# Performance work log

Measured on AMD Instinct MI355X. Metric: run time of the kernel, lower is better.

## Reference

```python
import jax, jax.numpy as jnp
import numpy as np

OUT_FEATURES = 4096
IN_FEATURES = 4096


def _unpack_int4_symmetric(packed, n_values):
    # packed: uint8-valued int32 array; each byte holds two 4-bit values:
    # high nibble first, low nibble second (packing was (v0 << 4) | v1 with v in [0,15]=q+8)
    high = (packed >> 4) & 15
    low = packed & 15
    interleaved = jnp.stack([high, low], axis=-1).reshape(-1)[:n_values]
    # symmetric: quantized value q = nibble - 8, zero_point = 0
    return interleaved.astype(jnp.float32) - 8.0


def setup_inputs() -> dict:
    key = jax.random.key(0)
    k1, k2, k3, k4, k5 = jax.random.split(key, 5)
    x = jax.random.normal(k1, (4, 2048, IN_FEATURES), dtype=jnp.float32)
    packed_w = jax.random.randint(k2, (OUT_FEATURES * IN_FEATURES // 2,), 0, 256, dtype=jnp.int32)
    packed_b = jax.random.randint(k3, (OUT_FEATURES // 2,), 0, 256, dtype=jnp.int32)
    scale_w = jax.random.uniform(k4, (), dtype=jnp.float32) * 0.01 + 1e-4
    scale_b = jax.random.uniform(k5, (), dtype=jnp.float32) * 0.01 + 1e-4
    return {"x": x, "packed_w": packed_w, "packed_b": packed_b,
            "scale_w": scale_w, "scale_b": scale_b}


def reference(x, packed_w, packed_b, scale_w, scale_b):
    # dequantize weight: scale * (q - zero_point), zero_point = 0 (symmetric)
    qw = _unpack_int4_symmetric(packed_w, OUT_FEATURES * IN_FEATURES)
    W = (scale_w * qw).reshape(OUT_FEATURES, IN_FEATURES)  # [O, I]
    qb = _unpack_int4_symmetric(packed_b, OUT_FEATURES)
    b = scale_b * qb  # [O]
    # F.linear(x, W, b) = x @ W.T + b
    return jnp.einsum('bsi,oi->bso', x, W) + b
```

## Files before the change

### kernel.cpp

```cpp
#include <hip/hip_runtime.h>

#define M_DIM 8192
#define N_DIM 4096
#define K_DIM 4096

typedef _Float16 f16;
typedef _Float16 f16x8 __attribute__((ext_vector_type(8)));
typedef float f32x16 __attribute__((ext_vector_type(16)));

__device__ __forceinline__ void lds_async16(void* lds, const void* g) {
    __builtin_amdgcn_global_load_lds(
        (const __attribute__((address_space(1))) void*)(void*)g,
        (__attribute__((address_space(3))) void*)lds, 16, 0, 0);
}

__global__ __launch_bounds__(256) void cvt_x_kernel(const float* __restrict__ x, f16* __restrict__ xh) {
    size_t idx  = (size_t)blockIdx.x * 256 + threadIdx.x;
    size_t base = idx * 8;
    const float4* xp = (const float4*)(x + base);
    float4 v0 = xp[0], v1 = xp[1];
    f16x8 h;
    h[0] = (f16)v0.x; h[1] = (f16)v0.y; h[2] = (f16)v0.z; h[3] = (f16)v0.w;
    h[4] = (f16)v1.x; h[5] = (f16)v1.y; h[6] = (f16)v1.z; h[7] = (f16)v1.w;
    *(f16x8*)(xh + base) = h;
}

__global__ __launch_bounds__(256) void cvt_w_kernel(const int* __restrict__ pw, f16* __restrict__ wh) {
    size_t idx = (size_t)blockIdx.x * 256 + threadIdx.x;
    int4 v = ((const int4*)pw)[idx];
    f16x8 h;
    int a;
    a = v.x; h[0] = (f16)(((a >> 4) & 15) - 8); h[1] = (f16)((a & 15) - 8);
    a = v.y; h[2] = (f16)(((a >> 4) & 15) - 8); h[3] = (f16)((a & 15) - 8);
    a = v.z; h[4] = (f16)(((a >> 4) & 15) - 8); h[5] = (f16)((a & 15) - 8);
    a = v.w; h[6] = (f16)(((a >> 4) & 15) - 8); h[7] = (f16)((a & 15) - 8);
    *(f16x8*)(wh + idx * 8) = h;
}

__global__ __launch_bounds__(512, 2) void gemm_f16(const f16* __restrict__ A, const f16* __restrict__ B,
                                                   const int* __restrict__ pb,
                                                   const float* __restrict__ psw, const float* __restrict__ psb,
                                                   float* __restrict__ out) {
    __shared__ f16 As[2][16384];
    __shared__ f16 Bs[2][16384];

    const int tid  = threadIdx.x;
    const int wave = tid >> 6;
    const int lane = tid & 63;
    const int l32  = lane & 31;
    const int half = lane >> 5;
    const int wm   = wave >> 2;
    const int wn   = wave & 3;

    const int bid = blockIdx.x;
    const int swz = (bid & 7) * 64 + (bid >> 3);
    const int bx  = swz & 15;
    const int by  = swz >> 4;
    const int mbase = by * 256;
    const int nbase = bx * 256;

    const int rL   = ((lane >> 5) & 1) * 8 + ((lane >> 2) & 7);
    const int kswz = (((lane & 3) ^ ((lane >> 3) & 3))) * 8;
    const f16* aSrc[2]; const f16* bSrc[2];
#pragma unroll
    for (int j = 0; j < 2; j++) {
        aSrc[j] = A + (size_t)(mbase + j * 128 + wave * 16 + rL) * K_DIM + kswz;
        bSrc[j] = B + (size_t)(nbase + j * 128 + wave * 16 + rL) * K_DIM + kswz;
    }
    const int dA0 = wave * 512;
    const int dA1 = 4096 + wave * 512;

    int aoff[4], axr[4];
#pragma unroll
    for (int mt = 0; mt < 4; mt++) {
        int ra = wm * 128 + mt * 32 + l32;
        aoff[mt] = (ra >> 3) * 256 + (ra & 7) * 32;
        axr[mt]  = ((ra & 7) >> 1) & 3;
    }
    int boff[2], bxr[2];
#pragma unroll
    for (int nt = 0; nt < 2; nt++) {
        int rb = wn * 64 + nt * 32 + l32;
        boff[nt] = (rb >> 3) * 256 + (rb & 7) * 32;
        bxr[nt]  = ((rb & 7) >> 1) & 3;
    }

    f32x16 acc[4][2] = {};

    lds_async16(&As[0][dA0], aSrc[0]);
    lds_async16(&As[0][dA1], aSrc[1]);
    lds_async16(&Bs[0][dA0], bSrc[0]);
    lds_async16(&Bs[0][dA1], bSrc[1]);
    lds_async16(&As[0][8192 + dA0], aSrc[0] + 32);
    lds_async16(&As[0][8192 + dA1], aSrc[1] + 32);
    lds_async16(&Bs[0][8192 + dA0], bSrc[0] + 32);
    lds_async16(&Bs[0][8192 + dA1], bSrc[1] + 32);
    asm volatile("s_waitcnt vmcnt(0)" ::: "memory");
    __builtin_amdgcn_s_barrier();

#pragma unroll 1
    for (int t = 0; t < 64; ++t) {
        const f16* Ac = As[t & 1];
        const f16* Bc = Bs[t & 1];
        f16* An = As[(t + 1) & 1];
        f16* Bn = Bs[(t + 1) & 1];
        const int kn = (t < 63 ? (t + 1) : 63) * 64;

        lds_async16(&An[dA0], aSrc[0] + kn);
        lds_async16(&An[dA1], aSrc[1] + kn);
        lds_async16(&Bn[dA0], bSrc[0] + kn);
        lds_async16(&Bn[dA1], bSrc[1] + kn);
        lds_async16(&An[8192 + dA0], aSrc[0] + kn + 32);
        lds_async16(&An[8192 + dA1], aSrc[1] + kn + 32);
        lds_async16(&Bn[8192 + dA0], bSrc[0] + kn + 32);
        lds_async16(&Bn[8192 + dA1], bSrc[1] + kn + 32);
        __builtin_amdgcn_sched_barrier(0);

#pragma unroll
        for (int kk = 0; kk < 4; ++kk) {
            const int h_   = kk >> 1;
            const int kc2_ = (kk & 1) * 2 + half;
            f16x8 af[4], bf[2];
#pragma unroll
            for (int mt = 0; mt < 4; mt++)
                af[mt] = *(const f16x8*)&Ac[h_ * 8192 + aoff[mt] + ((kc2_ ^ axr[mt]) << 3)];
#pragma unroll
            for (int nt = 0; nt < 2; nt++)
                bf[nt] = *(const f16x8*)&Bc[h_ * 8192 + boff[nt] + ((kc2_ ^ bxr[nt]) << 3)];
#pragma unroll
            for (int mt = 0; mt < 4; mt++)
#pragma unroll
                for (int nt = 0; nt < 2; nt++)
                    acc[mt][nt] = __builtin_amdgcn_mfma_f32_32x32x16_f16(af[mt], bf[nt], acc[mt][nt], 0, 0, 0);
        }

        asm volatile("s_waitcnt vmcnt(0)" ::: "memory");
        __builtin_amdgcn_s_barrier();
        __builtin_amdgcn_sched_barrier(0);
    }

    const float sw = *psw;
    const float sb = *psb;

#pragma unroll
    for (int nt = 0; nt < 2; nt++) {
        const int gcol = nbase + wn * 64 + nt * 32 + l32;
        const int p    = pb[gcol >> 1];
        const int nib  = (gcol & 1) ? (p & 15) : ((p >> 4) & 15);
        const float bias = sb * (float)(nib - 8);
#pragma unroll
        for (int mt = 0; mt < 4; mt++) {
            const int rbase = mbase + wm * 128 + mt * 32 + half * 4;
#pragma unroll
            for (int g = 0; g < 4; g++) {
                float* o = out + (size_t)(rbase + g * 8) * N_DIM + gcol;
#pragma unroll
                for (int r = 0; r < 4; r++)
                    o[(size_t)r * N_DIM] = sw * acc[mt][nt][g * 4 + r] + bias;
            }
        }
    }
}

__global__ __launch_bounds__(256) void gemm_fallback(const float* __restrict__ x, const int* __restrict__ pw,
                                                     const int* __restrict__ pb,
                                                     const float* __restrict__ psw, const float* __restrict__ psb,
                                                     float* __restrict__ out) {
    __shared__ float As[16][17];
    __shared__ float Bs[16][17];
    const int tx = threadIdx.x & 15, ty = threadIdx.x >> 4;
    const int row = blockIdx.y * 16 + ty;
    const int col = blockIdx.x * 16 + tx;
    float acc = 0.f;
    for (int k0 = 0; k0 < K_DIM; k0 += 16) {
        As[ty][tx] = x[(size_t)row * K_DIM + k0 + tx];
        const int nrow = blockIdx.x * 16 + ty;
        const int k = k0 + tx;
        const int p = pw[((size_t)nrow * K_DIM + k) >> 1];
        const int nib = (k & 1) ? (p & 15) : ((p >> 4) & 15);
        Bs[ty][tx] = (float)(nib - 8);
        __syncthreads();
#pragma unroll
        for (int kk = 0; kk < 16; kk++)
            acc += As[ty][kk] * Bs[tx][kk];
        __syncthreads();
    }
    const float sw = *psw, sb = *psb;
    const int p = pb[col >> 1];
    const int nib = (col & 1) ? (p & 15) : ((p >> 4) & 15);
    out[(size_t)row * N_DIM + col] = sw * acc + sb * (float)(nib - 8);
}

extern "C" void kernel_launch(void* const* d_in, const int* in_sizes, int n_in,
                              void* d_out, int out_size, void* d_ws, size_t ws_size,
                              hipStream_t stream) {
    (void)in_sizes; (void)n_in; (void)out_size;
    const float* x   = (const float*)d_in[0];
    const int*   pw  = (const int*)d_in[1];
    const int*   pb  = (const int*)d_in[2];
    const float* psw = (const float*)d_in[3];
    const float* psb = (const float*)d_in[4];
    float* out = (float*)d_out;

    const size_t xh_bytes = (size_t)M_DIM * K_DIM * sizeof(f16);
    const size_t wh_bytes = (size_t)N_DIM * K_DIM * sizeof(f16);

    if (ws_size >= xh_bytes + wh_bytes) {
        f16* xh = (f16*)d_ws;
        f16* wh = (f16*)((char*)d_ws + xh_bytes);
        cvt_x_kernel<<<(M_DIM * (size_t)K_DIM) / 8 / 256, 256, 0, stream>>>(x, xh);
        cvt_w_kernel<<<((size_t)N_DIM * K_DIM / 2) / 4 / 256, 256, 0, stream>>>(pw, wh);
        gemm_f16<<<dim3((M_DIM / 256) * (N_DIM / 256)), 512, 0, stream>>>(xh, wh, pb, psw, psb, out);
    } else {
        gemm_fallback<<<dim3(N_DIM / 16, M_DIM / 16), 256, 0, stream>>>(x, pw, pb, psw, psb, out);
    }
}
```

Measured before the change: 541.3 us.

## Restructure f16 GEMM main loop into four-phase pipelined schedule with 16x16 MFMA

Rewrites the GEMM inner loop to use 16x16x32 MFMA tiles and splits each K step into four quadrant phases. Global-to-LDS loads for the next tiles are interleaved between phases, with barriers and s_setprio raising priority around the MFMA bursts. Loads are issued per half-tile kind so copies overlap compute at a finer grain. Out-of-range stages load into a scratch buffer to keep vmcnt counts uniform. This adds more barriers per iteration and relies on exact waitcnt accounting, which could stall or be fragile.

```diff
diff --git a/kernel.cpp b/kernel.cpp
--- a/kernel.cpp
+++ b/kernel.cpp
@@ -6,7 +6,7 @@
 
 typedef _Float16 f16;
 typedef _Float16 f16x8 __attribute__((ext_vector_type(8)));
-typedef float f32x16 __attribute__((ext_vector_type(16)));
+typedef float f32x4 __attribute__((ext_vector_type(4)));
 
 __device__ __forceinline__ void lds_async16(void* lds, const void* g) {
     __builtin_amdgcn_global_load_lds(
@@ -41,16 +41,18 @@
                                                    const int* __restrict__ pb,
                                                    const float* __restrict__ psw, const float* __restrict__ psb,
                                                    float* __restrict__ out) {
-    __shared__ f16 As[2][16384];
-    __shared__ f16 Bs[2][16384];
+    __shared__ f16 AS[2][2][8192];
+    __shared__ f16 BS[2][2][8192];
+    __shared__ f16 SCR[1024];
 
     const int tid  = threadIdx.x;
-    const int wave = tid >> 6;
+    const int w    = tid >> 6;
     const int lane = tid & 63;
-    const int l32  = lane & 31;
-    const int half = lane >> 5;
-    const int wm   = wave >> 2;
-    const int wn   = wave & 3;
+    const int l16  = lane & 15;
+    const int lq   = lane >> 4;
+    const int wm   = w >> 2;
+    const int wn   = w & 3;
+    const int hb   = wn >> 1;
 
     const int bid = blockIdx.x;
     const int swz = (bid & 7) * 64 + (bid >> 3);
@@ -59,107 +61,166 @@
     const int mbase = by * 256;
     const int nbase = bx * 256;
 
-    const int rL   = ((lane >> 5) & 1) * 8 + ((lane >> 2) & 7);
-    const int kswz = (((lane & 3) ^ ((lane >> 3) & 3))) * 8;
-    const f16* aSrc[2]; const f16* bSrc[2];
-#pragma unroll
-    for (int j = 0; j < 2; j++) {
-        aSrc[j] = A + (size_t)(mbase + j * 128 + wave * 16 + rL) * K_DIM + kswz;
-        bSrc[j] = B + (size_t)(nbase + j * 128 + wave * 16 + rL) * K_DIM + kswz;
-    }
-    const int dA0 = wave * 512;
-    const int dA1 = 4096 + wave * 512;
-
-    int aoff[4], axr[4];
-#pragma unroll
-    for (int mt = 0; mt < 4; mt++) {
-        int ra = wm * 128 + mt * 32 + l32;
-        aoff[mt] = (ra >> 3) * 256 + (ra & 7) * 32;
-        axr[mt]  = ((ra & 7) >> 1) & 3;
-    }
-    int boff[2], bxr[2];
-#pragma unroll
-    for (int nt = 0; nt < 2; nt++) {
-        int rb = wn * 64 + nt * 32 + l32;
-        boff[nt] = (rb >> 3) * 256 + (rb & 7) * 32;
-        bxr[nt]  = ((rb & 7) >> 1) & 3;
-    }
-
-    f32x16 acc[4][2] = {};
-
-    lds_async16(&As[0][dA0], aSrc[0]);
-    lds_async16(&As[0][dA1], aSrc[1]);
-    lds_async16(&Bs[0][dA0], bSrc[0]);
-    lds_async16(&Bs[0][dA1], bSrc[1]);
-    lds_async16(&As[0][8192 + dA0], aSrc[0] + 32);
-    lds_async16(&As[0][8192 + dA1], aSrc[1] + 32);
-    lds_async16(&Bs[0][8192 + dA0], bSrc[0] + 32);
-    lds_async16(&Bs[0][8192 + dA1], bSrc[1] + 32);
+    const int uL = (lane & 7) ^ (((lane >> 5) & 1) << 1);
+    const f16* aSrc00 = A + (size_t)(mbase + w * 16 + (lane >> 3)) * K_DIM + uL * 8;
+    const f16* aSrc01 = aSrc00 + (size_t)8 * K_DIM;
+    const f16* aSrc10 = aSrc00 + (size_t)128 * K_DIM;
+    const f16* aSrc11 = aSrc10 + (size_t)8 * K_DIM;
+    const f16* bSrc00 = B + (size_t)(nbase + w * 16 + (lane >> 3)) * K_DIM + uL * 8;
+    const f16* bSrc01 = bSrc00 + (size_t)8 * K_DIM;
+    const f16* bSrc10 = bSrc00 + (size_t)128 * K_DIM;
+    const f16* bSrc11 = bSrc10 + (size_t)8 * K_DIM;
+    const int wb = w * 1024;
+
+#define STAGE_KIND(tidx, kind) do {                                                              \
+    if ((tidx) < 64) {                                                                           \
+        const int b_ = (tidx) & 1;                                                               \
+        if ((kind) == 0) { lds_async16(&AS[b_][0][wb], aSrc00 + (tidx) * 64);                    \
+                           lds_async16(&AS[b_][0][wb + 512], aSrc01 + (tidx) * 64); }            \
+        else if ((kind) == 1) { lds_async16(&BS[b_][0][wb], bSrc00 + (tidx) * 64);               \
+                                lds_async16(&BS[b_][0][wb + 512], bSrc01 + (tidx) * 64); }       \
+        else if ((kind) == 2) { lds_async16(&AS[b_][1][wb], aSrc10 + (tidx) * 64);               \
+                                lds_async16(&AS[b_][1][wb + 512], aSrc11 + (tidx) * 64); }       \
+        else { lds_async16(&BS[b_][1][wb], bSrc10 + (tidx) * 64);                                \
+               lds_async16(&BS[b_][1][wb + 512], bSrc11 + (tidx) * 64); }                        \
+    } else {                                                                                     \
+        lds_async16(&SCR[0], aSrc00 + 4032); lds_async16(&SCR[512], aSrc01 + 4032);              \
+    }                                                                                            \
+} while (0)
+
+    int aAd[2][4];
+#pragma unroll
+    for (int mq = 0; mq < 2; mq++)
+#pragma unroll
+        for (int fi = 0; fi < 4; fi++) {
+            const int r  = mq * 64 + fi * 16 + l16;
+            const int xr = ((r >> 2) & 1) << 1;
+            aAd[mq][fi]  = r * 64 + ((lq ^ xr) << 3);
+        }
+    int bAd[2][2];
+#pragma unroll
+    for (int nq = 0; nq < 2; nq++)
+#pragma unroll
+        for (int gi = 0; gi < 2; gi++) {
+            const int r  = (wn & 1) * 64 + nq * 32 + gi * 16 + l16;
+            const int xr = ((r >> 2) & 1) << 1;
+            bAd[nq][gi]  = r * 64 + ((lq ^ xr) << 3);
+        }
+
+    f32x4 acc[8][4] = {};
+
+    STAGE_KIND(0, 0); STAGE_KIND(0, 1); STAGE_KIND(0, 2); STAGE_KIND(0, 3);
+    STAGE_KIND(1, 1); STAGE_KIND(1, 0);
+    asm volatile("s_waitcnt vmcnt(4)" ::: "memory");
+    __builtin_amdgcn_s_barrier();
+
+#pragma unroll 1
+    for (int T = 0; T < 64; ++T) {
+        const int cb = T & 1;
+        const f16* Ah = &AS[cb][wm][0];
+        const f16* Bh = &BS[cb][hb][0];
+        f16x8 aF0[4][2], aF1[4][2], bF0[2][2], bF1[2][2];
+
+#pragma unroll
+        for (int fi = 0; fi < 4; fi++)
+#pragma unroll
+            for (int s = 0; s < 2; s++) aF0[fi][s] = *(const f16x8*)&Ah[aAd[0][fi] + s * 32];
+#pragma unroll
+        for (int gi = 0; gi < 2; gi++)
+#pragma unroll
+            for (int s = 0; s < 2; s++) bF0[gi][s] = *(const f16x8*)&Bh[bAd[0][gi] + s * 32];
+        STAGE_KIND(T + 1, 3);
+        asm volatile("s_waitcnt lgkmcnt(8)" ::: "memory");
+        __builtin_amdgcn_s_barrier();
+        asm volatile("s_waitcnt lgkmcnt(0)" ::: "memory");
+        __builtin_amdgcn_sched_barrier(0);
+        __builtin_amdgcn_s_setprio(1);
+#pragma unroll
+        for (int s = 0; s < 2; s++)
+#pragma unroll
+            for (int fi = 0; fi < 4; fi++)
+#pragma unroll
+                for (int gi = 0; gi < 2; gi++)
+                    acc[fi][gi] = __builtin_amdgcn_mfma_f32_16x16x32_f16(aF0[fi][s], bF0[gi][s], acc[fi][gi], 0, 0, 0);
+        __builtin_amdgcn_s_setprio(0);
+        __builtin_amdgcn_s_barrier();
+
+#pragma unroll
+        for (int gi = 0; gi < 2; gi++)
+#pragma unroll
+            for (int s = 0; s < 2; s++) bF1[gi][s] = *(const f16x8*)&Bh[bAd[1][gi] + s * 32];
+        STAGE_KIND(T + 1, 2);
+        __builtin_amdgcn_s_barrier();
+        asm volatile("s_waitcnt lgkmcnt(0)" ::: "memory");
+        __builtin_amdgcn_sched_barrier(0);
+        __builtin_amdgcn_s_setprio(1);
+#pragma unroll
+        for (int s = 0; s < 2; s++)
+#pragma unroll
+            for (int fi = 0; fi < 4; fi++)
+#pragma unroll
+                for (int gi = 0; gi < 2; gi++)
+                    acc[fi][2 + gi] = __builtin_amdgcn_mfma_f32_16x16x32_f16(aF0[fi][s], bF1[gi][s], acc[fi][2 + gi], 0, 0, 0);
+        __builtin_amdgcn_s_setprio(0);
+        __builtin_amdgcn_s_barrier();
+
+#pragma unroll
+        for (int fi = 0; fi < 4; fi++)
+#pragma unroll
+            for (int s = 0; s < 2; s++) aF1[fi][s] = *(const f16x8*)&Ah[aAd[1][fi] + s * 32];
+        STAGE_KIND(T + 2, 1);
+        __builtin_amdgcn_s_barrier();
+        asm volatile("s_waitcnt lgkmcnt(0)" ::: "memory");
+        __builtin_amdgcn_sched_barrier(0);
+        __builtin_amdgcn_s_setprio(1);
+#pragma unroll
+        for (int s = 0; s < 2; s++)
+#pragma unroll
+            for (int fi = 0; fi < 4; fi++)
+#pragma unroll
+                for (int gi = 0; gi < 2; gi++)
+                    acc[4 + fi][2 + gi] = __builtin_amdgcn_mfma_f32_16x16x32_f16(aF1[fi][s], bF1[gi][s], acc[4 + fi][2 + gi], 0, 0, 0);
+        __builtin_amdgcn_s_setprio(0);
+        __builtin_amdgcn_s_barrier();
+
+        STAGE_KIND(T + 2, 0);
+        __builtin_amdgcn_s_barrier();
+        asm volatile("s_waitcnt lgkmcnt(0)" ::: "memory");
+        __builtin_amdgcn_sched_barrier(0);
+        __builtin_amdgcn_s_setprio(1);
+#pragma unroll
+        for (int s = 0; s < 2; s++)
+#pragma unroll
+            for (int fi = 0; fi < 4; fi++)
+#pragma unroll
+                for (int gi = 0; gi < 2; gi++)
+                    acc[4 + fi][gi] = __builtin_amdgcn_mfma_f32_16x16x32_f16(aF1[fi][s], bF0[gi][s], acc[4 + fi][gi], 0, 0, 0);
+        __builtin_amdgcn_s_setprio(0);
+        asm volatile("s_waitcnt vmcnt(4)" ::: "memory");
+        __builtin_amdgcn_s_barrier();
+    }
+
     asm volatile("s_waitcnt vmcnt(0)" ::: "memory");
-    __builtin_amdgcn_s_barrier();
-
-#pragma unroll 1
-    for (int t = 0; t < 64; ++t) {
-        const f16* Ac = As[t & 1];
-        const f16* Bc = Bs[t & 1];
-        f16* An = As[(t + 1) & 1];
-        f16* Bn = Bs[(t + 1) & 1];
-        const int kn = (t < 63 ? (t + 1) : 63) * 64;
-
-        lds_async16(&An[dA0], aSrc[0] + kn);
-        lds_async16(&An[dA1], aSrc[1] + kn);
-        lds_async16(&Bn[dA0], bSrc[0] + kn);
-        lds_async16(&Bn[dA1], bSrc[1] + kn);
-        lds_async16(&An[8192 + dA0], aSrc[0] + kn + 32);
-        lds_async16(&An[8192 + dA1], aSrc[1] + kn + 32);
-        lds_async16(&Bn[8192 + dA0], bSrc[0] + kn + 32);
-        lds_async16(&Bn[8192 + dA1], bSrc[1] + kn + 32);
-        __builtin_amdgcn_sched_barrier(0);
-
-#pragma unroll
-        for (int kk = 0; kk < 4; ++kk) {
-            const int h_   = kk >> 1;
-            const int kc2_ = (kk & 1) * 2 + half;
-            f16x8 af[4], bf[2];
-#pragma unroll
-            for (int mt = 0; mt < 4; mt++)
-                af[mt] = *(const f16x8*)&Ac[h_ * 8192 + aoff[mt] + ((kc2_ ^ axr[mt]) << 3)];
-#pragma unroll
-            for (int nt = 0; nt < 2; nt++)
-                bf[nt] = *(const f16x8*)&Bc[h_ * 8192 + boff[nt] + ((kc2_ ^ bxr[nt]) << 3)];
-#pragma unroll
-            for (int mt = 0; mt < 4; mt++)
-#pragma unroll
-                for (int nt = 0; nt < 2; nt++)
-                    acc[mt][nt] = __builtin_amdgcn_mfma_f32_32x32x16_f16(af[mt], bf[nt], acc[mt][nt], 0, 0, 0);
-        }
-
-        asm volatile("s_waitcnt vmcnt(0)" ::: "memory");
-        __builtin_amdgcn_s_barrier();
-        __builtin_amdgcn_sched_barrier(0);
-    }
 
     const float sw = *psw;
     const float sb = *psb;
 
 #pragma unroll
-    for (int nt = 0; nt < 2; nt++) {
-        const int gcol = nbase + wn * 64 + nt * 32 + l32;
+    for (int gj = 0; gj < 4; gj++) {
+        const int gcol = nbase + wn * 64 + gj * 16 + l16;
         const int p    = pb[gcol >> 1];
         const int nib  = (gcol & 1) ? (p & 15) : ((p >> 4) & 15);
         const float bias = sb * (float)(nib - 8);
 #pragma unroll
-        for (int mt = 0; mt < 4; mt++) {
-            const int rbase = mbase + wm * 128 + mt * 32 + half * 4;
-#pragma unroll
-            for (int g = 0; g < 4; g++) {
-                float* o = out + (size_t)(rbase + g * 8) * N_DIM + gcol;
-#pragma unroll
-                for (int r = 0; r < 4; r++)
-                    o[(size_t)r * N_DIM] = sw * acc[mt][nt][g * 4 + r] + bias;
-            }
+        for (int fi = 0; fi < 8; fi++) {
+            const int grow = mbase + wm * 128 + fi * 16 + lq * 4;
+            float* o = out + (size_t)grow * N_DIM + gcol;
+#pragma unroll
+            for (int r = 0; r < 4; r++)
+                o[(size_t)r * N_DIM] = sw * acc[fi][gj][r] + bias;
         }
     }
+#undef STAGE_KIND
 }
 
 __global__ __launch_bounds__(256) void gemm_fallback(const float* __restrict__ x, const int* __restrict__ pw,
```

New measurement: 547.6 us. No clear change (+1.2%).
